# Performance work log

Measured on AMD Instinct MI355X. Metric: run time of the kernel, lower is better.

The kernel has to match this reference:

```python
import jax, jax.numpy as jnp
import numpy as np

NB_BINS = 10
N = 33554432  # number of predictions


def setup_inputs() -> dict:
    key = jax.random.key(0)
    k1, k2 = jax.random.split(key)
    logits = jax.random.normal(k1, (N,), dtype=jnp.float32)
    labels = jax.random.randint(k2, (N,), 0, 2, dtype=jnp.int32)
    return {"logits": logits, "labels": labels}


def reference(logits, labels):
    nb = NB_BINS
    conf = jax.nn.sigmoid(logits)
    # Bin b covers (b/nb, (b+1)/nb]: conf > lower & conf <= upper.
    # ceil(conf*nb)-1 maps exact boundary k/nb to bin k-1, matching gt/le.
    # sigmoid output is strictly in (0,1) for finite logits, so clip is safe.
    bins = jnp.clip(jnp.ceil(conf * nb).astype(jnp.int32) - 1, 0, nb - 1)

    counts = jax.ops.segment_sum(jnp.ones_like(conf), bins, num_segments=nb)
    label_sum = jax.ops.segment_sum(labels.astype(conf.dtype), bins, num_segments=nb)
    conf_sum = jax.ops.segment_sum(conf, bins, num_segments=nb)

    nonempty = counts > 0
    denom = jnp.where(nonempty, counts, 1.0)
    positives_per_bin = jnp.where(nonempty, label_sum / denom, 0.0)
    confidence_per_bin = jnp.where(nonempty, conf_sum / denom, 0.0)

    ece_i = jnp.where(nonempty, jnp.abs(positives_per_bin - confidence_per_bin), 0.0)
    ece = jnp.sum(ece_i)
    max_ece = jnp.max(ece_i)  # original inits max_ece=0, zeros for empty bins match
    return positives_per_bin, confidence_per_bin, ece, max_ece
```

## Files before the change

### kernel.cpp

```cpp
#include <hip/hip_runtime.h>

#define NB 10
#define BLOCK 256
#define GRID 2048


typedef float vfloat4 __attribute__((ext_vector_type(4)));
typedef int   vint4   __attribute__((ext_vector_type(4)));

__device__ __forceinline__ void acc_one(float xx, unsigned ll,
                                        unsigned long long& cnt64,
                                        unsigned long long& lab64,
                                        unsigned long long& rA,
                                        unsigned long long& rB) {
    float e = __expf(-xx);
    float conf = __builtin_amdgcn_rcpf(1.0f + e);
    float t = conf * 10.0f;
    int b = (int)t;
    b = min(b, NB - 1);
    float r = t - (float)b;
    unsigned rfix = (unsigned)__builtin_fmaf(r, 63.0f, 0.5f);
    int s6 = b * 6;
    cnt64 += 1ULL << s6;
    lab64 += (unsigned long long)ll << s6;
    bool hi = b >= 5;
    int s12 = (hi ? b - 5 : b) * 12;
    unsigned long long val = (unsigned long long)rfix << s12;
    rA += hi ? 0ULL : val;
    rB += hi ? val : 0ULL;
}

__device__ __forceinline__ void flush_packed(unsigned long long& cnt64,
                                             unsigned long long& lab64,
                                             unsigned long long& rA,
                                             unsigned long long& rB,
                                             unsigned* cl, unsigned* ru) {
#pragma unroll
    for (int i = 0; i < NB; ++i) {
        unsigned c = (unsigned)((cnt64 >> (6 * i)) & 63ULL);
        unsigned l = (unsigned)((lab64 >> (6 * i)) & 63ULL);
        cl[i] += c | (l << 16);
    }
#pragma unroll
    for (int i = 0; i < 5; ++i) {
        ru[i]     += (unsigned)((rA >> (12 * i)) & 4095ULL);
        ru[5 + i] += (unsigned)((rB >> (12 * i)) & 4095ULL);
    }
    cnt64 = 0ULL; lab64 = 0ULL; rA = 0ULL; rB = 0ULL;
}

__global__ __launch_bounds__(BLOCK) void ece_partial(const float* __restrict__ logits,
                                                     const int* __restrict__ labels,
                                                     unsigned int* __restrict__ ws,
                                                     int n, int wstride) {
    const int tid = threadIdx.x;
    const int gtid = blockIdx.x * BLOCK + tid;
    const int n4 = n >> 2;
    const int S = GRID * BLOCK;
    const vfloat4* __restrict__ l4 = (const vfloat4*)logits;
    const vint4*   __restrict__ b4 = (const vint4*)labels;

    unsigned cl[NB], ru[NB];
#pragma unroll
    for (int i = 0; i < NB; ++i) { cl[i] = 0u; ru[i] = 0u; }

    int v = gtid;
    while (v < n4) {
        unsigned long long cnt64 = 0ULL, lab64 = 0ULL, rA = 0ULL, rB = 0ULL;
        int done = 0;
        while (done < 8 && v + 3 * S < n4) {
            vfloat4 x0 = __builtin_nontemporal_load(&l4[v]);
            vfloat4 x1 = __builtin_nontemporal_load(&l4[v + S]);
            vfloat4 x2 = __builtin_nontemporal_load(&l4[v + 2 * S]);
            vfloat4 x3 = __builtin_nontemporal_load(&l4[v + 3 * S]);
            vint4   y0 = __builtin_nontemporal_load(&b4[v]);
            vint4   y1 = __builtin_nontemporal_load(&b4[v + S]);
            vint4   y2 = __builtin_nontemporal_load(&b4[v + 2 * S]);
            vint4   y3 = __builtin_nontemporal_load(&b4[v + 3 * S]);
            v += 4 * S;
            done += 4;
#pragma unroll
            for (int j = 0; j < 4; ++j) acc_one(x0[j], (unsigned)y0[j], cnt64, lab64, rA, rB);
#pragma unroll
            for (int j = 0; j < 4; ++j) acc_one(x1[j], (unsigned)y1[j], cnt64, lab64, rA, rB);
#pragma unroll
            for (int j = 0; j < 4; ++j) acc_one(x2[j], (unsigned)y2[j], cnt64, lab64, rA, rB);
#pragma unroll
            for (int j = 0; j < 4; ++j) acc_one(x3[j], (unsigned)y3[j], cnt64, lab64, rA, rB);
        }
        while (done < 8 && v < n4) {
            vfloat4 x = __builtin_nontemporal_load(&l4[v]);
            vint4   y = __builtin_nontemporal_load(&b4[v]);
            v += S;
            done += 1;
#pragma unroll
            for (int j = 0; j < 4; ++j) acc_one(x[j], (unsigned)y[j], cnt64, lab64, rA, rB);
        }
        flush_packed(cnt64, lab64, rA, rB, cl, ru);
    }
    if (gtid == 0 && (n & 3)) {
        unsigned long long cnt64 = 0ULL, lab64 = 0ULL, rA = 0ULL, rB = 0ULL;
        for (int j2 = n4 * 4; j2 < n; ++j2) {
            acc_one(__builtin_nontemporal_load(&logits[j2]),
                    (unsigned)__builtin_nontemporal_load(&labels[j2]),
                    cnt64, lab64, rA, rB);
        }
        flush_packed(cnt64, lab64, rA, rB, cl, ru);
    }

#pragma unroll
    for (int i = 0; i < NB; ++i) {
#pragma unroll
        for (int off = 32; off > 0; off >>= 1) {
            cl[i] += __shfl_down(cl[i], off, 64);
            ru[i] += __shfl_down(ru[i], off, 64);
        }
    }

    __shared__ unsigned red[4][2 * NB];
    const int wave = tid >> 6, lane = tid & 63;
    if (lane == 0) {
#pragma unroll
        for (int i = 0; i < NB; ++i) { red[wave][i] = cl[i]; red[wave][NB + i] = ru[i]; }
    }
    __syncthreads();
    if (tid < 2 * NB) {
        unsigned s = red[0][tid] + red[1][tid] + red[2][tid] + red[3][tid];
        if (tid < NB) {
            atomicAdd(&ws[tid * wstride], s & 0xffffu);
            atomicAdd(&ws[(NB + tid) * wstride], s >> 16);
        } else {
            atomicAdd(&ws[(NB + tid) * wstride], s);
        }
    }
}

__global__ void ece_final(const unsigned int* __restrict__ ws, float* __restrict__ out,
                          int wstride) {
    if (threadIdx.x == 0 && blockIdx.x == 0) {
        float ece = 0.0f, mx = 0.0f;
        for (int b = 0; b < NB; ++b) {
            unsigned cnt = ws[b * wstride];
            unsigned lab = ws[(NB + b) * wstride];
            unsigned rs  = ws[(2 * NB + b) * wstride];
            float pos = 0.0f, cfb = 0.0f, e = 0.0f;
            if (cnt > 0u) {
                float inv = 1.0f / (float)cnt;
                pos = (float)lab * inv;
                cfb = ((float)b + (float)rs * (1.0f / 63.0f) * inv) * 0.1f;
                e = fabsf(pos - cfb);
            }
            out[b] = pos;
            out[NB + b] = cfb;
            ece += e;
            mx = fmaxf(mx, e);
        }
        out[2 * NB] = ece;
        out[2 * NB + 1] = mx;
    }
}

extern "C" void kernel_launch(void* const* d_in, const int* in_sizes, int n_in,
                              void* d_out, int out_size, void* d_ws, size_t ws_size,
                              hipStream_t stream) {
    const float* logits = (const float*)d_in[0];
    const int*   labels = (const int*)d_in[1];
    float* out = (float*)d_out;
    unsigned int* ws = (unsigned int*)d_ws;
    int n = in_sizes[0];

    int wstride = (ws_size >= 30 * 16 * sizeof(unsigned)) ? 16 : 1;
    hipMemsetAsync(d_ws, 0, (size_t)(30 * wstride) * sizeof(unsigned), stream);

    ece_partial<<<GRID, BLOCK, 0, stream>>>(logits, labels, ws, n, wstride);
    ece_final<<<1, 64, 0, stream>>>(ws, out, wstride);
}
```

Measured before the change: 279.8 us.

## Switch to block-contiguous tiles with all loads issued before compute

Replaces the grid-strided access (four loads per step, strided by the whole grid) with block-contiguous tiles of K=8 float4/int4 per thread. All 16 loads are issued up front before any compute, and the grid doubles to 4096 blocks. The aim is more memory-level parallelism per thread and better DRAM locality per block. In exchange it uses more registers per thread, which may lower occupancy, and launches more blocks that each do a separate atomic flush.

```diff
diff --git a/kernel.cpp b/kernel.cpp
--- a/kernel.cpp
+++ b/kernel.cpp
@@ -2,7 +2,8 @@
 
 #define NB 10
 #define BLOCK 256
-#define GRID 2048
+#define GRID 4096
+#define K 8
 
 
 typedef float vfloat4 __attribute__((ext_vector_type(4)));
@@ -54,9 +55,7 @@
                                                      unsigned int* __restrict__ ws,
                                                      int n, int wstride) {
     const int tid = threadIdx.x;
-    const int gtid = blockIdx.x * BLOCK + tid;
     const int n4 = n >> 2;
-    const int S = GRID * BLOCK;
     const vfloat4* __restrict__ l4 = (const vfloat4*)logits;
     const vint4*   __restrict__ b4 = (const vint4*)labels;
 
@@ -64,47 +63,41 @@
 #pragma unroll
     for (int i = 0; i < NB; ++i) { cl[i] = 0u; ru[i] = 0u; }
 
-    int v = gtid;
-    while (v < n4) {
+    const int TILE = BLOCK * K;
+    for (int tbase = blockIdx.x * TILE; tbase < n4; tbase += GRID * TILE) {
         unsigned long long cnt64 = 0ULL, lab64 = 0ULL, rA = 0ULL, rB = 0ULL;
-        int done = 0;
-        while (done < 8 && v + 3 * S < n4) {
-            vfloat4 x0 = __builtin_nontemporal_load(&l4[v]);
-            vfloat4 x1 = __builtin_nontemporal_load(&l4[v + S]);
-            vfloat4 x2 = __builtin_nontemporal_load(&l4[v + 2 * S]);
-            vfloat4 x3 = __builtin_nontemporal_load(&l4[v + 3 * S]);
-            vint4   y0 = __builtin_nontemporal_load(&b4[v]);
-            vint4   y1 = __builtin_nontemporal_load(&b4[v + S]);
-            vint4   y2 = __builtin_nontemporal_load(&b4[v + 2 * S]);
-            vint4   y3 = __builtin_nontemporal_load(&b4[v + 3 * S]);
-            v += 4 * S;
-            done += 4;
+        if (tbase + TILE <= n4) {
+            vfloat4 x[K];
+            vint4   y[K];
+            const int base = tbase + tid;
 #pragma unroll
-            for (int j = 0; j < 4; ++j) acc_one(x0[j], (unsigned)y0[j], cnt64, lab64, rA, rB);
+            for (int k = 0; k < K; ++k) x[k] = __builtin_nontemporal_load(&l4[base + k * BLOCK]);
 #pragma unroll
-            for (int j = 0; j < 4; ++j) acc_one(x1[j], (unsigned)y1[j], cnt64, lab64, rA, rB);
+            for (int k = 0; k < K; ++k) y[k] = __builtin_nontemporal_load(&b4[base + k * BLOCK]);
 #pragma unroll
-            for (int j = 0; j < 4; ++j) acc_one(x2[j], (unsigned)y2[j], cnt64, lab64, rA, rB);
+            for (int k = 0; k < K; ++k) {
 #pragma unroll
-            for (int j = 0; j < 4; ++j) acc_one(x3[j], (unsigned)y3[j], cnt64, lab64, rA, rB);
-        }
-        while (done < 8 && v < n4) {
-            vfloat4 x = __builtin_nontemporal_load(&l4[v]);
-            vint4   y = __builtin_nontemporal_load(&b4[v]);
-            v += S;
-            done += 1;
+                for (int j = 0; j < 4; ++j)
+                    acc_one(x[k][j], (unsigned)y[k][j], cnt64, lab64, rA, rB);
+            }
+        } else {
+            for (int k = 0; k < K; ++k) {
+                int idx = tbase + tid + k * BLOCK;
+                if (idx < n4) {
+                    vfloat4 x = __builtin_nontemporal_load(&l4[idx]);
+                    vint4   yv = __builtin_nontemporal_load(&b4[idx]);
 #pragma unroll
-            for (int j = 0; j < 4; ++j) acc_one(x[j], (unsigned)y[j], cnt64, lab64, rA, rB);
+                    for (int j = 0; j < 4; ++j)
+                        acc_one(x[j], (unsigned)yv[j], cnt64, lab64, rA, rB);
+                }
+            }
         }
         flush_packed(cnt64, lab64, rA, rB, cl, ru);
     }
-    if (gtid == 0 && (n & 3)) {
+    if (blockIdx.x == 0 && tid == 0 && (n & 3)) {
         unsigned long long cnt64 = 0ULL, lab64 = 0ULL, rA = 0ULL, rB = 0ULL;
-        for (int j2 = n4 * 4; j2 < n; ++j2) {
-            acc_one(__builtin_nontemporal_load(&logits[j2]),
-                    (unsigned)__builtin_nontemporal_load(&labels[j2]),
-                    cnt64, lab64, rA, rB);
-        }
+        for (int j2 = n4 * 4; j2 < n; ++j2)
+            acc_one(logits[j2], (unsigned)labels[j2], cnt64, lab64, rA, rB);
         flush_packed(cnt64, lab64, rA, rB, cl, ru);
     }
 
```

New measurement: 302.5 us. +8.1%, slower.
